# Optimization experiments

Measured on AMD Instinct MI355X. Metric: run time of the kernel, lower is better.

The kernel has to match this reference:

```python
import jax, jax.numpy as jnp
import numpy as np

B, S, D, H, DF, L, V, MAXLEN = 8, 1024, 768, 12, 3072, 6, 32000, 2048
HD = D // H
EPS = 1e-5

def _pe(max_length, d_model):
    position = jnp.arange(max_length, dtype=jnp.float32)[:, None]
    i = jnp.arange(d_model, dtype=jnp.float32)[None, :]
    angles = position * (1.0 / jnp.power(10000.0, 2.0 * jnp.floor(i / 2.0) / d_model))
    pe = jnp.zeros((max_length, d_model), dtype=jnp.float32)
    pe = pe.at[:, 0::2].set(jnp.sin(angles[:, 0::2]))
    pe = pe.at[:, 1::2].set(jnp.cos(angles[:, 1::2]))
    return pe

def _layernorm(x, g, b):
    mu = jnp.mean(x, axis=-1, keepdims=True)
    var = jnp.mean((x - mu) ** 2, axis=-1, keepdims=True)
    return (x - mu) * jax.lax.rsqrt(var + EPS) * g + b

def setup_inputs() -> dict:
    key = jax.random.key(0)
    ks = jax.random.split(key, 16)
    s = 0.02
    emb = jax.random.normal(ks[0], (V, D), jnp.float32) * s
    emb = emb.at[0].set(0.0)  # padding_idx=0
    inp = {
        'input_ids': jax.random.randint(ks[1], (B, S), 0, V),
        'emb': emb,
        'pe': _pe(MAXLEN, D),
        'Wq': jax.random.normal(ks[2], (L, D, D), jnp.float32) * s,
        'bq': jnp.zeros((L, D), jnp.float32),
        'Wk': jax.random.normal(ks[3], (L, D, D), jnp.float32) * s,
        'bk': jnp.zeros((L, D), jnp.float32),
        'Wv': jax.random.normal(ks[4], (L, D, D), jnp.float32) * s,
        'bv': jnp.zeros((L, D), jnp.float32),
        'W1': jax.random.normal(ks[5], (L, DF, D), jnp.float32) * s,
        'b1': jnp.zeros((L, DF), jnp.float32),
        'W2': jax.random.normal(ks[6], (L, D, DF), jnp.float32) * s,
        'b2': jnp.zeros((L, D), jnp.float32),
        'ln1_g': jnp.ones((L, D), jnp.float32),
        'ln1_b': jnp.zeros((L, D), jnp.float32),
        'ln2_g': jnp.ones((L, D), jnp.float32),
        'ln2_b': jnp.zeros((L, D), jnp.float32),
    }
    return inp

def _mha(x, Wq, bq, Wk, bk, Wv, bv):
    b, s, _ = x.shape
    q = (x @ Wq.T + bq).reshape(b, H, s, HD)  # faithful to torch .view (no transpose)
    k = (x @ Wk.T + bk).reshape(b, H, s, HD)
    v = (x @ Wv.T + bv).reshape(b, H, s, HD)
    scores = jnp.einsum('bhqd,bhkd->bhqk', q, k) / (HD ** 0.5)
    att = jax.nn.softmax(scores, axis=-1)
    o = jnp.einsum('bhqk,bhkd->bhqd', att, v)
    return o.transpose(0, 2, 1, 3).reshape(b, s, D)

def reference(input_ids, emb, pe, Wq, bq, Wk, bk, Wv, bv, W1, b1, W2, b2, ln1_g, ln1_b, ln2_g, ln2_b):
    x = emb[input_ids] + pe[:input_ids.shape[1], :]
    # dropout is identity in eval mode
    for l in range(L):
        h1 = _mha(x, Wq[l], bq[l], Wk[l], bk[l], Wv[l], bv[l])
        y1 = _layernorm(x + h1, ln1_g[l], ln1_b[l])
        h2 = jax.nn.relu(y1 @ W1[l].T + b1[l]) @ W2[l].T + b2[l]
        x = _layernorm(y1 + h2, ln2_g[l], ln2_b[l])
    return x
```

## Files before the change

kernel.cpp:

```cpp
#include <hip/hip_runtime.h>


typedef _Float16 f16;
typedef _Float16 half4 __attribute__((ext_vector_type(4)));
typedef _Float16 half8 __attribute__((ext_vector_type(8)));
typedef float f32x4 __attribute__((ext_vector_type(4)));
typedef float f32x16 __attribute__((ext_vector_type(16)));

constexpr int Bn = 8, Sn = 1024, Dn = 768, Hn = 12, HDn = 64, DFn = 3072, Ln = 6;
constexpr int BS = Bn * Sn;

__device__ __forceinline__ void glds16(const f16* g, f16* l) {
  __builtin_amdgcn_global_load_lds(
      (const __attribute__((address_space(1))) unsigned int*)g,
      (__attribute__((address_space(3))) unsigned int*)l, 16, 0, 0);
}

__device__ __forceinline__ float ex2(float x) {
#if __has_builtin(__builtin_amdgcn_exp2f)
  return __builtin_amdgcn_exp2f(x);
#else
  return exp2f(x);
#endif
}

__global__ __launch_bounds__(256) void pack_qkv(
    const float* __restrict__ Wq, const float* __restrict__ Wk, const float* __restrict__ Wv,
    const float* __restrict__ bq, const float* __restrict__ bk, const float* __restrict__ bv,
    f16* __restrict__ Wo, float* __restrict__ bo) {
  const long per = (long)Dn * Dn;
  const long t = (long)blockIdx.x * 256 + threadIdx.x;
  const long totalW4 = (long)Ln * 3 * per / 4;
  if (t < totalW4) {
    const long i = t * 4;
    const int l = (int)(i / (3 * per));
    long rem = i - (long)l * 3 * per;
    const int which = (int)(rem / per);
    const long e = rem - (long)which * per;
    const float* s = (which == 0) ? Wq : ((which == 1) ? Wk : Wv);
    const float4 v = *(const float4*)&s[(long)l * per + e];
    half4 h = {(f16)v.x, (f16)v.y, (f16)v.z, (f16)v.w};
    *(half4*)&Wo[i] = h;
  }
  if (t < (long)Ln * 3 * Dn) {
    int l = (int)(t / (3 * Dn));
    int rem = (int)(t % (3 * Dn));
    int which = rem / Dn, c = rem % Dn;
    const float* s = (which == 0) ? bq : ((which == 1) ? bk : bv);
    bo[t] = s[l * Dn + c];
  }
}

__global__ __launch_bounds__(256) void f32_to_f16_k(
    const float* __restrict__ src, f16* __restrict__ dst, long n) {
  long i = ((long)blockIdx.x * 256 + threadIdx.x) * 4;
  if (i < n) {
    float4 v = *(const float4*)&src[i];
    half4 h = {(f16)v.x, (f16)v.y, (f16)v.z, (f16)v.w};
    *(half4*)&dst[i] = h;
  }
}

__global__ __launch_bounds__(256) void embed_k(
    const int* __restrict__ ids, const float* __restrict__ emb, const float* __restrict__ pe,
    float* __restrict__ Xf, f16* __restrict__ Xh) {
  const int row = blockIdx.x;
  const int s = row & (Sn - 1);
  const int id = ids[row];
  const size_t eb = (size_t)id * Dn, pb = (size_t)s * Dn, ob = (size_t)row * Dn;
  for (int c = threadIdx.x; c < Dn; c += 256) {
    float v = emb[eb + c] + pe[pb + c];
    Xf[ob + c] = v;
    Xh[ob + c] = (f16)v;
  }
}

template <int MODE>
__global__ __launch_bounds__(256) void gemm_bt(
    const f16* __restrict__ A, const f16* __restrict__ Bw, const float* __restrict__ bias,
    float* __restrict__ outF, f16* __restrict__ o0, f16* __restrict__ o1, f16* __restrict__ o2,
    int M, int N, int K, int lda) {
  const int m0 = blockIdx.x * 128;
  const int n0 = blockIdx.y * 128;
  const int tid = threadIdx.x;
  const int lane = tid & 63, wave = tid >> 6;
  const int wm = wave & 1, wn = wave >> 1;
  const int l15 = lane & 15, l4 = lane >> 4;

  constexpr int SLOT = 128 * 32;
  __shared__ __align__(16) f16 As[3 * SLOT];
  __shared__ __align__(16) f16 Bs[3 * SLOT];

  const f32x4 z4 = {0.f, 0.f, 0.f, 0.f};
  f32x4 acc[4][4];
#pragma unroll
  for (int i = 0; i < 4; i++)
#pragma unroll
    for (int j = 0; j < 4; j++) acc[i][j] = z4;

  const int sRow = wave * 32 + (lane >> 2);
  const int sCol = (lane & 3) * 8;
  const int kz = (MODE == 4) ? ((int)blockIdx.z * K) : 0;
  const f16* gA = A + (size_t)(m0 + sRow) * lda + kz + sCol;
  const f16* gB = Bw + (size_t)(n0 + sRow) * lda + kz + sCol;
  f16* lA = &As[(wave * 32) * 32];
  f16* lB = &Bs[(wave * 32) * 32];
  const size_t rowStep = (size_t)16 * lda;

  auto stage = [&](int buf, int k0) {
    glds16(gA + k0, lA + buf * SLOT);
    glds16(gA + k0 + rowStep, lA + buf * SLOT + 16 * 32);
    glds16(gB + k0, lB + buf * SLOT);
    glds16(gB + k0 + rowStep, lB + buf * SLOT + 16 * 32);
  };

  const int NT = K / 32;
  stage(0, 0);
  stage(1, 32);

  const int kr = 8 * l4;
  int cur = 0, nxt2 = 2;
  for (int t = 0; t < NT; ++t) {
    if (t + 1 < NT) {
      asm volatile("s_waitcnt vmcnt(4)" ::: "memory");
    } else {
      asm volatile("s_waitcnt vmcnt(0)" ::: "memory");
    }
    __builtin_amdgcn_sched_barrier(0);
    __builtin_amdgcn_s_barrier();
    __builtin_amdgcn_sched_barrier(0);

    if (t + 2 < NT) stage(nxt2, (t + 2) * 32);

    half8 af[4], bfr[4];
#pragma unroll
    for (int i = 0; i < 4; i++)
      af[i] = *(const half8*)&As[cur * SLOT + (wm * 64 + i * 16 + l15) * 32 + kr];
#pragma unroll
    for (int j = 0; j < 4; j++)
      bfr[j] = *(const half8*)&Bs[cur * SLOT + (wn * 64 + j * 16 + l15) * 32 + kr];
#pragma unroll
    for (int i = 0; i < 4; i++)
#pragma unroll
      for (int j = 0; j < 4; j++)
        acc[i][j] = __builtin_amdgcn_mfma_f32_16x16x32_f16(af[i], bfr[j], acc[i][j], 0, 0, 0);

    cur = (cur == 2) ? 0 : cur + 1;
    nxt2 = (nxt2 == 2) ? 0 : nxt2 + 1;
  }

  const int colb = n0 + wn * 64;
  const int rowb = m0 + wm * 64;
#pragma unroll
  for (int j = 0; j < 4; j++) {
    const int col = colb + j * 16 + l15;
    const float bb = (MODE == 4) ? 0.f : bias[col];
#pragma unroll
    for (int i = 0; i < 4; i++) {
      const int rb = rowb + i * 16 + l4 * 4;
#pragma unroll
      for (int r = 0; r < 4; r++) {
        float v = acc[i][j][r] + bb;
        const int row = rb + r;
        if (MODE == 1) {
          v = fmaxf(v, 0.f);
          o0[(size_t)row * N + col] = (f16)v;
        } else if (MODE == 3) {
          const int sel = col / 768;
          const int cl = col - sel * 768;
          f16* op = (sel == 0) ? o0 : ((sel == 1) ? o1 : o2);
          op[(size_t)row * 768 + cl] = (f16)v;
        } else if (MODE == 4) {
          outF[((size_t)blockIdx.z * M + row) * N + col] = v;
        } else {
          o0[(size_t)row * N + col] = (f16)v;
        }
      }
    }
  }
}

__global__ __launch_bounds__(256, 3) void attn_k(
    const f16* __restrict__ Qg, const f16* __restrict__ Kg, const f16* __restrict__ Vg,
    float* __restrict__ O) {
  const int bh = blockIdx.x;
  const int q0 = blockIdx.y * 128;
  const int b = bh / Hn, h = bh - b * Hn;
  const size_t base = (size_t)b * (Sn * Dn) + (size_t)h * (Sn * HDn);
  const f16* Qh = Qg + base;
  const f16* Kh = Kg + base;
  const f16* Vh = Vg + base;

  const int tid = threadIdx.x, lane = tid & 63, wave = tid >> 6;
  const int l31 = lane & 31;
  const int hi = lane >> 5;

  __shared__ __align__(16) f16 Ks[64 * 72];
  __shared__ __align__(16) f16 Vt[64 * 72];

  const int qrow = q0 + wave * 32 + l31;
  half8 qf[4];
#pragma unroll
  for (int m = 0; m < 4; m++)
    qf[m] = *(const half8*)&Qh[(size_t)qrow * HDn + 16 * m + 8 * hi];

  f32x16 Oacc0, Oacc1;
#pragma unroll
  for (int i = 0; i < 16; i++) { Oacc0[i] = 0.f; Oacc1[i] = 0.f; }
  float mrow = -1e30f, lrow = 0.f;
  const float csc = 0.18033688011112042f;

  for (int kt = 0; kt < Sn / 64; ++kt) {
#pragma unroll
    for (int cc = 0; cc < 2; cc++) {
      const int c = tid + cc * 256;
      const int row = c >> 3, col = (c & 7) * 8;
      *(int4*)&Ks[row * 72 + col] = *(const int4*)&Kh[(size_t)(kt * 64 + row) * HDn + col];
    }
#pragma unroll
    for (int ee = 0; ee < 2; ee++) {
      const int e = tid + ee * 256;
      const int hd = e & 63, kpo = e >> 6;
      f16 tmp[8];
#pragma unroll
      for (int j = 0; j < 8; j++)
        tmp[j] = Vh[(size_t)(kt * 64 + kpo * 8 + j) * HDn + hd];
      *(int4*)&Vt[hd * 72 + kpo * 8] = *(const int4*)tmp;
    }
    __syncthreads();

    f32x16 s0, s1;
#pragma unroll
    for (int i = 0; i < 16; i++) { s0[i] = 0.f; s1[i] = 0.f; }
#pragma unroll
    for (int m = 0; m < 4; m++) {
      half8 k0 = *(const half8*)&Ks[l31 * 72 + 16 * m + 8 * hi];
      half8 k1 = *(const half8*)&Ks[(32 + l31) * 72 + 16 * m + 8 * hi];
      s0 = __builtin_amdgcn_mfma_f32_32x32x16_f16(k0, qf[m], s0, 0, 0, 0);
      s1 = __builtin_amdgcn_mfma_f32_32x32x16_f16(k1, qf[m], s1, 0, 0, 0);
    }

    float t8[8];
#pragma unroll
    for (int i = 0; i < 8; i++)
      t8[i] = fmaxf(fmaxf(s0[i], s0[i + 8]), fmaxf(s1[i], s1[i + 8]));
#pragma unroll
    for (int i = 0; i < 4; i++) t8[i] = fmaxf(t8[i], t8[i + 4]);
    float mx = fmaxf(fmaxf(t8[0], t8[1]), fmaxf(t8[2], t8[3]));
    mx = fmaxf(mx, __shfl_xor(mx, 32));
    const float M = fmaxf(mrow, mx * csc);
    const float alpha = ex2(mrow - M);

#pragma unroll
    for (int i = 0; i < 16; i++) {
      s0[i] = ex2(fmaf(s0[i], csc, -M));
      s1[i] = ex2(fmaf(s1[i], csc, -M));
    }
    float r0 = 0.f, r1 = 0.f, r2 = 0.f, r3 = 0.f;
#pragma unroll
    for (int i = 0; i < 16; i += 4) {
      r0 += s0[i]; r1 += s0[i + 1]; r2 += s0[i + 2]; r3 += s0[i + 3];
      r0 += s1[i]; r1 += s1[i + 1]; r2 += s1[i + 2]; r3 += s1[i + 3];
    }
    float rsum = (r0 + r1) + (r2 + r3);
    rsum += __shfl_xor(rsum, 32);
    lrow = lrow * alpha + rsum;
    mrow = M;
#pragma unroll
    for (int i = 0; i < 16; i++) { Oacc0[i] *= alpha; Oacc1[i] *= alpha; }

    unsigned pA[2][4], pB[2][4];
#pragma unroll
    for (int t = 0; t < 4; t++) {
      pA[0][t] = __builtin_bit_cast(unsigned, __builtin_amdgcn_cvt_pkrtz(s0[4 * t + 0], s0[4 * t + 1]));
      pB[0][t] = __builtin_bit_cast(unsigned, __builtin_amdgcn_cvt_pkrtz(s0[4 * t + 2], s0[4 * t + 3]));
      pA[1][t] = __builtin_bit_cast(unsigned, __builtin_amdgcn_cvt_pkrtz(s1[4 * t + 0], s1[4 * t + 1]));
      pB[1][t] = __builtin_bit_cast(unsigned, __builtin_amdgcn_cvt_pkrtz(s1[4 * t + 2], s1[4 * t + 3]));
    }

#pragma unroll
    for (int c = 0; c < 4; c++) {
      const int g = c >> 1, tt = 2 * (c & 1);
      const unsigned ownA = hi ? pA[g][tt + 1] : pA[g][tt];
      const unsigned ownB = hi ? pB[g][tt + 1] : pB[g][tt];
      const unsigned sndA = hi ? pA[g][tt] : pA[g][tt + 1];
      const unsigned sndB = hi ? pB[g][tt] : pB[g][tt + 1];
      const unsigned rA = (unsigned)__shfl_xor((int)sndA, 32);
      const unsigned rB = (unsigned)__shfl_xor((int)sndB, 32);
      int4 w;
      w.x = (int)(hi ? rA : ownA);
      w.y = (int)(hi ? rB : ownB);
      w.z = (int)(hi ? ownA : rA);
      w.w = (int)(hi ? ownB : rB);
      const half8 pf = __builtin_bit_cast(half8, w);
      const half8 v0 = *(const half8*)&Vt[l31 * 72 + 16 * c + 8 * hi];
      const half8 v1 = *(const half8*)&Vt[(32 + l31) * 72 + 16 * c + 8 * hi];
      Oacc0 = __builtin_amdgcn_mfma_f32_32x32x16_f16(v0, pf, Oacc0, 0, 0, 0);
      Oacc1 = __builtin_amdgcn_mfma_f32_32x32x16_f16(v1, pf, Oacc1, 0, 0, 0);
    }
    __syncthreads();
  }

  const float inv = 1.f / lrow;
  float* Orow = O + ((size_t)b * Sn + qrow) * Dn + h * HDn;
#pragma unroll
  for (int t = 0; t < 4; t++) {
    float4 o0, o1;
    o0.x = Oacc0[4 * t + 0] * inv; o0.y = Oacc0[4 * t + 1] * inv;
    o0.z = Oacc0[4 * t + 2] * inv; o0.w = Oacc0[4 * t + 3] * inv;
    o1.x = Oacc1[4 * t + 0] * inv; o1.y = Oacc1[4 * t + 1] * inv;
    o1.z = Oacc1[4 * t + 2] * inv; o1.w = Oacc1[4 * t + 3] * inv;
    *(float4*)&Orow[8 * t + 4 * hi] = o0;
    *(float4*)&Orow[32 + 8 * t + 4 * hi] = o1;
  }
}

__global__ __launch_bounds__(256) void add_ln(
    const float* __restrict__ Xi, const float* __restrict__ Hr,
    const float* __restrict__ g, const float* __restrict__ bt,
    float* __restrict__ Yf, f16* __restrict__ Yh) {
  const int row = blockIdx.x;
  const int tid = threadIdx.x;
  const size_t base = (size_t)row * Dn;
  float v0 = Xi[base + tid] + Hr[base + tid];
  float v1 = Xi[base + tid + 256] + Hr[base + tid + 256];
  float v2 = Xi[base + tid + 512] + Hr[base + tid + 512];

  __shared__ float red[8];
  float s = v0 + v1 + v2;
  for (int off = 32; off; off >>= 1) s += __shfl_down(s, off);
  const int wv = tid >> 6, ln = tid & 63;
  if (ln == 0) red[wv] = s;
  __syncthreads();
  if (tid == 0) red[4] = (red[0] + red[1] + red[2] + red[3]) * (1.f / Dn);
  __syncthreads();
  const float mu = red[4];
  const float d0 = v0 - mu, d1 = v1 - mu, d2 = v2 - mu;
  float vs = d0 * d0 + d1 * d1 + d2 * d2;
  for (int off = 32; off; off >>= 1) vs += __shfl_down(vs, off);
  if (ln == 0) red[wv] = vs;
  __syncthreads();
  if (tid == 0) red[5] = rsqrtf((red[0] + red[1] + red[2] + red[3]) * (1.f / Dn) + 1e-5f);
  __syncthreads();
  const float rs = red[5];
  float y0 = d0 * rs * g[tid] + bt[tid];
  float y1 = d1 * rs * g[tid + 256] + bt[tid + 256];
  float y2 = d2 * rs * g[tid + 512] + bt[tid + 512];
  Yf[base + tid] = y0;        Yh[base + tid] = (f16)y0;
  Yf[base + tid + 256] = y1;  Yh[base + tid + 256] = (f16)y1;
  Yf[base + tid + 512] = y2;  Yh[base + tid + 512] = (f16)y2;
}

__global__ __launch_bounds__(256) void add_ln_sk2(
    const float* __restrict__ Xi, const float* __restrict__ P,
    const float* __restrict__ b2, const float* __restrict__ g, const float* __restrict__ bt,
    float* __restrict__ Yf, f16* __restrict__ Yh) {
  const int row = blockIdx.x;
  const int tid = threadIdx.x;
  const size_t base = (size_t)row * Dn;
  const size_t cs = (size_t)BS * Dn;
  float v0 = Xi[base + tid]       + P[base + tid]       + P[cs + base + tid]       + b2[tid];
  float v1 = Xi[base + tid + 256] + P[base + tid + 256] + P[cs + base + tid + 256] + b2[tid + 256];
  float v2 = Xi[base + tid + 512] + P[base + tid + 512] + P[cs + base + tid + 512] + b2[tid + 512];

  __shared__ float red[8];
  float s = v0 + v1 + v2;
  for (int off = 32; off; off >>= 1) s += __shfl_down(s, off);
  const int wv = tid >> 6, ln = tid & 63;
  if (ln == 0) red[wv] = s;
  __syncthreads();
  if (tid == 0) red[4] = (red[0] + red[1] + red[2] + red[3]) * (1.f / Dn);
  __syncthreads();
  const float mu = red[4];
  const float d0 = v0 - mu, d1 = v1 - mu, d2 = v2 - mu;
  float vs = d0 * d0 + d1 * d1 + d2 * d2;
  for (int off = 32; off; off >>= 1) vs += __shfl_down(vs, off);
  if (ln == 0) red[wv] = vs;
  __syncthreads();
  if (tid == 0) red[5] = rsqrtf((red[0] + red[1] + red[2] + red[3]) * (1.f / Dn) + 1e-5f);
  __syncthreads();
  const float rs = red[5];
  float y0 = d0 * rs * g[tid] + bt[tid];
  float y1 = d1 * rs * g[tid + 256] + bt[tid + 256];
  float y2 = d2 * rs * g[tid + 512] + bt[tid + 512];
  Yf[base + tid] = y0;        Yh[base + tid] = (f16)y0;
  Yf[base + tid + 256] = y1;  Yh[base + tid + 256] = (f16)y1;
  Yf[base + tid + 512] = y2;  Yh[base + tid + 512] = (f16)y2;
}

extern "C" void kernel_launch(void* const* d_in, const int* in_sizes, int n_in,
                              void* d_out, int out_size, void* d_ws, size_t ws_size,
                              hipStream_t stream) {
  const int* ids  = (const int*)d_in[0];
  const float* emb = (const float*)d_in[1];
  const float* pe  = (const float*)d_in[2];
  const float* Wq  = (const float*)d_in[3];
  const float* bq  = (const float*)d_in[4];
  const float* Wk  = (const float*)d_in[5];
  const float* bk  = (const float*)d_in[6];
  const float* Wv  = (const float*)d_in[7];
  const float* bv  = (const float*)d_in[8];
  const float* W1  = (const float*)d_in[9];
  const float* b1  = (const float*)d_in[10];
  const float* W2  = (const float*)d_in[11];
  const float* b2  = (const float*)d_in[12];
  const float* g1  = (const float*)d_in[13];
  const float* be1 = (const float*)d_in[14];
  const float* g2  = (const float*)d_in[15];
  const float* be2 = (const float*)d_in[16];
  float* out = (float*)d_out;

  char* w = (char*)d_ws;
  auto alloc = [&](size_t bytes) {
    char* p = w;
    w += (bytes + 255) & ~(size_t)255;
    return p;
  };
  f16* Wqkv  = (f16*)alloc((size_t)Ln * 3 * Dn * Dn * 2);
  float* bqkv = (float*)alloc((size_t)Ln * 3 * Dn * 4);
  f16* W1h   = (f16*)alloc((size_t)Ln * DFn * Dn * 2);
  f16* W2h   = (f16*)alloc((size_t)Ln * Dn * DFn * 2);
  float* Xf  = (float*)alloc((size_t)BS * Dn * 4);
  f16* Xh    = (f16*)alloc((size_t)BS * Dn * 2);
  f16* Qh    = (f16*)alloc((size_t)BS * Dn * 2);
  f16* Kh    = (f16*)alloc((size_t)BS * Dn * 2);
  f16* Vh    = (f16*)alloc((size_t)BS * Dn * 2);
  float* Of  = (float*)alloc((size_t)BS * Dn * 4);
  float* Y1f = (float*)alloc((size_t)BS * Dn * 4);
  f16* Y1h   = (f16*)alloc((size_t)BS * Dn * 2);
  f16* F1h   = (f16*)alloc((size_t)BS * DFn * 2);

  float* Pf = (float*)Qh;

  {
    const long totalW4 = (long)Ln * 3 * Dn * Dn / 4;
    const int gw = (int)((totalW4 + 255) / 256);
    pack_qkv<<<gw, 256, 0, stream>>>(Wq, Wk, Wv, bq, bk, bv, Wqkv, bqkv);
    const long n1 = (long)Ln * DFn * Dn;
    const int gc = (int)(n1 / 4 / 256);
    f32_to_f16_k<<<gc, 256, 0, stream>>>(W1, W1h, n1);
    f32_to_f16_k<<<gc, 256, 0, stream>>>(W2, W2h, n1);
  }

  embed_k<<<BS, 256, 0, stream>>>(ids, emb, pe, Xf, Xh);

  for (int l = 0; l < Ln; ++l) {
    gemm_bt<3><<<dim3(BS / 128, (3 * Dn) / 128), 256, 0, stream>>>(
        Xh, Wqkv + (size_t)l * 3 * Dn * Dn, bqkv + l * 3 * Dn,
        nullptr, Qh, Kh, Vh, BS, 3 * Dn, Dn, Dn);

    attn_k<<<dim3(Bn * Hn, Sn / 128), 256, 0, stream>>>(Qh, Kh, Vh, Of);

    add_ln<<<BS, 256, 0, stream>>>(Xf, Of, g1 + l * Dn, be1 + l * Dn, Y1f, Y1h);

    gemm_bt<1><<<dim3(BS / 128, DFn / 128), 256, 0, stream>>>(
        Y1h, W1h + (size_t)l * DFn * Dn, b1 + l * DFn,
        nullptr, F1h, nullptr, nullptr, BS, DFn, Dn, Dn);

    gemm_bt<4><<<dim3(BS / 128, Dn / 128, 2), 256, 0, stream>>>(
        F1h, W2h + (size_t)l * Dn * DFn, nullptr,
        Pf, nullptr, nullptr, nullptr, BS, Dn, DFn / 2, DFn);

    float* dstF = (l == Ln - 1) ? out : Xf;
    add_ln_sk2<<<BS, 256, 0, stream>>>(Y1f, Pf, b2 + l * Dn,
                                       g2 + l * Dn, be2 + l * Dn, dstF, Xh);
  }
}
```

Before: 1.823 ms.

## Use per-wave private LDS tiles, drop block barriers, and remap workgroups across XCDs

Each wave now stages its own 64-row slices of A and B into a private double-buffered LDS region, so the per-iteration workgroup barrier goes away and each wave only waits on its own vmcnt. Workgroup IDs are permuted in strides of eight so neighbouring tiles land on the same XCD, for better L2 locality. The MFMA block runs at raised priority, and launch bounds now request two blocks per CU. The cost is that waves sharing a row or column fetch the same tile separately, doubling global and LDS load traffic, and LDS use per block grows to 64KB.

```diff
diff --git a/kernel.cpp b/kernel.cpp
--- a/kernel.cpp
+++ b/kernel.cpp
@@ -76,20 +76,30 @@
 }
 
 template <int MODE>
-__global__ __launch_bounds__(256) void gemm_bt(
+__global__ __launch_bounds__(256, 2) void gemm_bt(
     const f16* __restrict__ A, const f16* __restrict__ Bw, const float* __restrict__ bias,
     float* __restrict__ outF, f16* __restrict__ o0, f16* __restrict__ o1, f16* __restrict__ o2,
     int M, int N, int K, int lda) {
-  const int m0 = blockIdx.x * 128;
-  const int n0 = blockIdx.y * 128;
+  const int gx = gridDim.x, gy = gridDim.y;
+  const int nwg = gx * gy * gridDim.z;
+  int lin = blockIdx.x + gx * (blockIdx.y + gy * blockIdx.z);
+  lin = (lin & 7) * (nwg >> 3) + (lin >> 3);
+  const int bx = lin % gx;
+  const int by = (lin / gx) % gy;
+  const int bz = lin / (gx * gy);
+
+  const int m0 = bx * 128;
+  const int n0 = by * 128;
   const int tid = threadIdx.x;
   const int lane = tid & 63, wave = tid >> 6;
   const int wm = wave & 1, wn = wave >> 1;
   const int l15 = lane & 15, l4 = lane >> 4;
 
-  constexpr int SLOT = 128 * 32;
-  __shared__ __align__(16) f16 As[3 * SLOT];
-  __shared__ __align__(16) f16 Bs[3 * SLOT];
+  constexpr int WREG = 2 * 2 * 64 * 32;
+  constexpr int SREG = 2 * 64 * 32;
+  constexpr int BOFF = 64 * 32;
+  __shared__ __align__(16) f16 S[4 * WREG];
+  f16* Wb = &S[wave * WREG];
 
   const f32x4 z4 = {0.f, 0.f, 0.f, 0.f};
   f32x4 acc[4][4];
@@ -98,20 +108,20 @@
 #pragma unroll
     for (int j = 0; j < 4; j++) acc[i][j] = z4;
 
-  const int sRow = wave * 32 + (lane >> 2);
+  const int sRow = lane >> 2;
   const int sCol = (lane & 3) * 8;
-  const int kz = (MODE == 4) ? ((int)blockIdx.z * K) : 0;
-  const f16* gA = A + (size_t)(m0 + sRow) * lda + kz + sCol;
-  const f16* gB = Bw + (size_t)(n0 + sRow) * lda + kz + sCol;
-  f16* lA = &As[(wave * 32) * 32];
-  f16* lB = &Bs[(wave * 32) * 32];
+  const int kz = (MODE == 4) ? (bz * K) : 0;
+  const f16* gA = A + (size_t)(m0 + wm * 64 + sRow) * lda + kz + sCol;
+  const f16* gB = Bw + (size_t)(n0 + wn * 64 + sRow) * lda + kz + sCol;
   const size_t rowStep = (size_t)16 * lda;
 
-  auto stage = [&](int buf, int k0) {
-    glds16(gA + k0, lA + buf * SLOT);
-    glds16(gA + k0 + rowStep, lA + buf * SLOT + 16 * 32);
-    glds16(gB + k0, lB + buf * SLOT);
-    glds16(gB + k0 + rowStep, lB + buf * SLOT + 16 * 32);
+  auto stage = [&](int slot, int k0) {
+    f16* d = Wb + slot * SREG;
+#pragma unroll
+    for (int r = 0; r < 4; r++) {
+      glds16(gA + k0 + r * rowStep, d + r * (16 * 32));
+      glds16(gB + k0 + r * rowStep, d + BOFF + r * (16 * 32));
+    }
   };
 
   const int NT = K / 32;
@@ -119,34 +129,32 @@
   stage(1, 32);
 
   const int kr = 8 * l4;
-  int cur = 0, nxt2 = 2;
   for (int t = 0; t < NT; ++t) {
+    f16* cb = Wb + (t & 1) * SREG;
     if (t + 1 < NT) {
-      asm volatile("s_waitcnt vmcnt(4)" ::: "memory");
+      asm volatile("s_waitcnt vmcnt(8)" ::: "memory");
     } else {
       asm volatile("s_waitcnt vmcnt(0)" ::: "memory");
     }
     __builtin_amdgcn_sched_barrier(0);
-    __builtin_amdgcn_s_barrier();
-    __builtin_amdgcn_sched_barrier(0);
-
-    if (t + 2 < NT) stage(nxt2, (t + 2) * 32);
-
-    half8 af[4], bfr[4];
+
+    half8 af[4], bf[4];
 #pragma unroll
     for (int i = 0; i < 4; i++)
-      af[i] = *(const half8*)&As[cur * SLOT + (wm * 64 + i * 16 + l15) * 32 + kr];
+      af[i] = *(const half8*)&cb[(i * 16 + l15) * 32 + kr];
 #pragma unroll
     for (int j = 0; j < 4; j++)
-      bfr[j] = *(const half8*)&Bs[cur * SLOT + (wn * 64 + j * 16 + l15) * 32 + kr];
+      bf[j] = *(const half8*)&cb[BOFF + (j * 16 + l15) * 32 + kr];
+
+    __builtin_amdgcn_s_setprio(1);
 #pragma unroll
     for (int i = 0; i < 4; i++)
 #pragma unroll
       for (int j = 0; j < 4; j++)
-        acc[i][j] = __builtin_amdgcn_mfma_f32_16x16x32_f16(af[i], bfr[j], acc[i][j], 0, 0, 0);
-
-    cur = (cur == 2) ? 0 : cur + 1;
-    nxt2 = (nxt2 == 2) ? 0 : nxt2 + 1;
+        acc[i][j] = __builtin_amdgcn_mfma_f32_16x16x32_f16(af[i], bf[j], acc[i][j], 0, 0, 0);
+    __builtin_amdgcn_s_setprio(0);
+
+    if (t + 2 < NT) stage(t & 1, (t + 2) * 32);
   }
 
   const int colb = n0 + wn * 64;
@@ -171,7 +179,7 @@
           f16* op = (sel == 0) ? o0 : ((sel == 1) ? o1 : o2);
           op[(size_t)row * 768 + cl] = (f16)v;
         } else if (MODE == 4) {
-          outF[((size_t)blockIdx.z * M + row) * N + col] = v;
+          outF[((size_t)bz * M + row) * N + col] = v;
         } else {
           o0[(size_t)row * N + col] = (f16)v;
         }
```

Result: slower. 2.214 ms (+21.5%).
